# Performance work log

Hardware: AMD Instinct MI355X
Metric: run time of the kernel (lower is better)

Reference implementation:

```python
import jax, jax.numpy as jnp
import numpy as np

NINP, NHID, NOUT = 400, 600, 400
HS = NHID + NOUT          # h_size = nhid + nout
NLEVELS, K, AUX_FREQ = 40, 2, 20
DILATION = [1]


def setup_inputs() -> dict:
    key = jax.random.key(0)
    ks = jax.random.split(key, 6)
    B, T = 8, 256
    bound = 0.01  # matches init_weights normal_(0, 0.01)
    return {
        "X": jax.random.normal(ks[0], (B, NINP, T), jnp.float32),
        "hid": jax.random.normal(ks[1], (B, HS, 1), jnp.float32),
        "cell": jax.random.normal(ks[2], (B, HS, 1), jnp.float32),
        "w1": jax.random.normal(ks[3], (4 * HS, NINP, K), jnp.float32) * bound,
        "w2": jax.random.normal(ks[4], (4 * HS, HS, K), jnp.float32) * bound,
        "b2": jax.random.normal(ks[5], (4 * HS,), jnp.float32) * bound,
    }


def _conv1d(x, w, d):
    # x: [B, Cin, T_padded], w: [Cout, Cin, K] -> [B, Cout, T]
    return jax.lax.conv_general_dilated(
        x, w, window_strides=(1,), padding='VALID', rhs_dilation=(d,),
        dimension_numbers=('NCH', 'OIH', 'NCH'))


def _forward(X, hid, cell, w1, w2, b2):
    B, _, T = X.shape
    ht = jnp.zeros((B, HS, T), X.dtype)
    ct = jnp.zeros((B, HS, T), X.dtype)

    # Input-side convolution is weight-tied and X never changes across levels,
    # so (like the torch dict cache) compute it once per distinct dilation.
    conv1 = {}
    for d in set(DILATION):
        pad = (K - 1) * d
        xp = jnp.pad(X, ((0, 0), (0, 0), (pad, 0)))
        conv1[d] = _conv1d(xp, w1, d)

    aux = []
    for i in range(NLEVELS):
        d = DILATION[i % len(DILATION)]
        pad = (K - 1) * d
        # causal left-pad of the hidden stream, filled with the initial hid
        z1 = jnp.concatenate([jnp.broadcast_to(hid, (B, HS, pad)), ht], axis=2)
        out = conv1[d] + _conv1d(z1, w2, d) + b2[None, :, None]  # [B, 4*HS, T]
        # shifted cell state, first d steps filled with the initial cell
        ct_1 = jnp.concatenate(
            [jnp.broadcast_to(cell, (B, HS, d)), ct[:, :, :-d]], axis=2)
        it = jax.nn.sigmoid(out[:, :HS])
        ot = jax.nn.sigmoid(out[:, HS:2 * HS])
        gt = jnp.tanh(out[:, 2 * HS:3 * HS])
        ft = jax.nn.sigmoid(out[:, 3 * HS:])
        ct = ft * ct_1 + it * gt
        ht = ot * jnp.tanh(ct)
        if i % AUX_FREQ == AUX_FREQ - 1:
            aux.append(ht[:, -NOUT:])  # [B, nout, T]

    out_main = jnp.transpose(ht[:, -NOUT:], (0, 2, 1))            # [B, T, nout]
    hc = (ht[:, :, -1:], ct[:, :, -1:])                            # ([B,HS,1], [B,HS,1])
    aux_outs = jnp.transpose(jnp.stack(aux, axis=0), (1, 0, 3, 2))  # [B, n_aux, T, nout]
    return out_main, hc, aux_outs


def reference(X, hid, cell, w1, w2, b2):
    return _forward(X, hid, cell, w1, w2, b2)
```

## Files before the change

### kernel.cpp

```cpp
#include <hip/hip_runtime.h>
#include <hip/hip_bf16.h>
#include <math.h>

typedef __bf16 bf16;
typedef __bf16 bf16x8 __attribute__((ext_vector_type(8)));
typedef __bf16 bf16x4 __attribute__((ext_vector_type(4)));
typedef float f32x4 __attribute__((ext_vector_type(4)));
typedef unsigned int u32;
typedef u32 u32x4 __attribute__((ext_vector_type(4)));

#define NINP 400
#define HS   1000
#define HP   1024
#define B_   8
#define T_   256
#define NT   2048
#define K2   2048
#define K1   1024
#define M_   4096

#define HT_OFF   819200
#define CT_OFF   827200
#define AUX_OFF  835200

typedef __attribute__((address_space(1))) const void gvoid;
typedef __attribute__((address_space(3))) void lvoid;

__device__ __forceinline__ void async_copy16(void* lds, const void* g) {
  __builtin_amdgcn_global_load_lds((gvoid*)g, (lvoid*)lds, 16, 0, 0);
}

__device__ __forceinline__ float sigm(float x) { return 1.0f / (1.0f + expf(-x)); }


__global__ void repack_w1(const float* __restrict__ w1, bf16* __restrict__ W1q) {
  int idx = blockIdx.x * 256 + threadIdx.x;
  if (idx >= M_ * K1) return;
  int pm = idx >> 10, k = idx & 1023;
  int g = (pm >> 4) & 3;
  int h = (pm >> 7) * 32 + ((pm >> 6) & 1) * 16 + (pm & 15);
  float v = 0.0f;
  if (h < HS) {
    int c = g * HS + h;
    if (k < 512) { if (k < NINP) v = w1[(size_t)c * (NINP * 2) + k * 2 + 0]; }
    else { int j = k - 512; if (j < NINP) v = w1[(size_t)c * (NINP * 2) + j * 2 + 1]; }
  }
  W1q[idx] = (bf16)v;
}

__global__ void repack_w2(const float* __restrict__ w2, bf16* __restrict__ W2q) {
  int idx = blockIdx.x * 256 + threadIdx.x;
  if (idx >= M_ * K2) return;
  int pm = idx >> 11, k = idx & 2047;
  int g = (pm >> 4) & 3;
  int h = (pm >> 7) * 32 + ((pm >> 6) & 1) * 16 + (pm & 15);
  float v = 0.0f;
  if (h < HS) {
    int c = g * HS + h;
    if (k < HP) { if (k < HS) v = w2[(size_t)c * (HS * 2) + k * 2 + 0]; }
    else { int j = k - HP; if (j < HS) v = w2[(size_t)c * (HS * 2) + j * 2 + 1]; }
  }
  W2q[idx] = (bf16)v;
}

__global__ void build_xt(const float* __restrict__ X, bf16* __restrict__ XT) {
  int idx = blockIdx.x * 256 + threadIdx.x;
  if (idx >= NT * K1) return;
  int n = idx >> 10, k = idx & 1023;
  int b = n >> 8, t = n & (T_ - 1);
  float v = 0.0f;
  if (k < 512) { if (k < NINP && t > 0) v = X[((size_t)b * NINP + k) * T_ + t - 1]; }
  else { int j = k - 512; if (j < NINP) v = X[((size_t)b * NINP + j) * T_ + t]; }
  XT[idx] = (bf16)v;
}

__global__ void build_hc(const float* __restrict__ hid, const float* __restrict__ cell,
                         bf16* __restrict__ hidp, float* __restrict__ cellp) {
  int idx = blockIdx.x * 256 + threadIdx.x;
  if (idx >= B_ * HP) return;
  int b = idx >> 10, k = idx & (HP - 1);
  hidp[idx]  = (k < HS) ? (bf16)hid[b * HS + k] : (bf16)0.0f;
  cellp[idx] = (k < HS) ? cell[b * HS + k] : 0.0f;
}


template <bool GATED>
__global__ __launch_bounds__(512, 2) void gemm_step(
    const bf16* __restrict__ A,
    const bf16* __restrict__ Bsrc,
    const bf16* __restrict__ hidp,
    const bf16* __restrict__ CbIn,
    bf16* __restrict__ CbOut,
    const float* __restrict__ b2,
    const bf16* __restrict__ ctprev,
    const float* __restrict__ cellp,
    bf16* __restrict__ ctnew,
    bf16* __restrict__ Hnew,
    int K) {
  __shared__ bf16 As[3][256][64];
  __shared__ bf16 Bs[3][128][64];

  const int tid = threadIdx.x;
  const int lane = tid & 63;
  const int w = tid >> 6;
  const int mh = w >> 1;
  const int nh = w & 1;
  const int dr = lane >> 3, c8 = lane & 7;
  const int swo = ((c8 - dr) & 7) * 8;
  const int quad = lane >> 4, col = lane & 15;

  const int L = blockIdx.y * 16 + blockIdx.x;
  const int bm = (L & 7) * 2 + (L >> 7);
  const int n0 = ((L >> 3) & 15) * 128;

  bf16x4 cb0[4], cb1[4], cb2[4], cb3[4];
  if (GATED) {
#pragma unroll
    for (int nt = 0; nt < 4; ++nt) {
      const int n = n0 + nh * 64 + nt * 16 + col;
      const size_t cb = (size_t)n * 4096 + (size_t)(bm * 256 + mh * 64) + quad * 4;
      cb0[nt] = *(const bf16x4*)&CbIn[cb + 0];
      cb1[nt] = *(const bf16x4*)&CbIn[cb + 16];
      cb2[nt] = *(const bf16x4*)&CbIn[cb + 32];
      cb3[nt] = *(const bf16x4*)&CbIn[cb + 48];
    }
  }

  f32x4 acc[4][4];
#pragma unroll
  for (int i = 0; i < 4; ++i)
#pragma unroll
    for (int j = 0; j < 4; ++j) acc[i][j] = (f32x4){0.f, 0.f, 0.f, 0.f};

  auto stage = [&](int buf, int it2) {
    const int k0 = it2 << 6;
#pragma unroll
    for (int i = 0; i < 4; ++i) {
      const int r = i * 64 + w * 8 + dr;
      async_copy16(&As[buf][i * 64 + w * 8][0],
                   A + (size_t)(bm * 256 + r) * K + k0 + swo);
    }
#pragma unroll
    for (int j = 0; j < 2; ++j) {
      const int r = j * 64 + w * 8 + dr;
      const int n = n0 + r;
      const bf16* bp;
      if (GATED) {
        const int kk = (k0 & (HP - 1)) + swo;
        if (k0 < HP) {
          const int t = n & (T_ - 1);
          bp = (t == 0) ? (hidp + (size_t)(n >> 8) * HP + kk)
                        : (Bsrc + (size_t)(n - 1) * HP + kk);
        } else {
          bp = Bsrc + (size_t)n * HP + kk;
        }
      } else {
        bp = Bsrc + (size_t)n * K + k0 + swo;
      }
      async_copy16(&Bs[buf][j * 64 + w * 8][0], bp);
    }
  };

  const int NIT = K >> 6;
  stage(0, 0);
  stage(1, 1);
  int cur = 0;
  for (int it = 0; it < NIT; ++it) {
    if (it + 1 < NIT) asm volatile("s_waitcnt vmcnt(6)" ::: "memory");
    else              asm volatile("s_waitcnt vmcnt(0)" ::: "memory");
    __builtin_amdgcn_s_barrier();
    if (it + 2 < NIT) {
      int nx = cur + 2; if (nx >= 3) nx -= 3;
      stage(nx, it + 2);
    }
#pragma unroll
    for (int kc = 0; kc < 64; kc += 32) {
      bf16x8 av[4], bv[4];
#pragma unroll
      for (int mt = 0; mt < 4; ++mt) {
        const int rA = mh * 64 + mt * 16 + col;
        av[mt] = *(const bf16x8*)&As[cur][rA][(((kc >> 3) + quad + rA) & 7) * 8];
      }
#pragma unroll
      for (int nt = 0; nt < 4; ++nt) {
        const int rB = nh * 64 + nt * 16 + col;
        bv[nt] = *(const bf16x8*)&Bs[cur][rB][(((kc >> 3) + quad + rB) & 7) * 8];
      }
      __builtin_amdgcn_s_setprio(1);
#pragma unroll
      for (int mt = 0; mt < 4; ++mt)
#pragma unroll
        for (int nt = 0; nt < 4; ++nt)
          acc[mt][nt] = __builtin_amdgcn_mfma_f32_16x16x32_bf16(av[mt], bv[nt], acc[mt][nt], 0, 0, 0);
      __builtin_amdgcn_s_setprio(0);
    }
    cur = (cur == 2) ? 0 : cur + 1;
  }
  __syncthreads();

  if (!GATED) {
    bf16 (*Csh)[256] = (bf16(*)[256])&As[0][0][0];
#pragma unroll
    for (int mt = 0; mt < 4; ++mt) {
#pragma unroll
      for (int nt = 0; nt < 4; ++nt) {
        const int nloc = nh * 64 + nt * 16 + col;
        bf16x4 v;
#pragma unroll
        for (int j = 0; j < 4; ++j) {
          const int h = bm * 64 + mh * 16 + quad * 4 + j;
          const float bias = (h < HS) ? b2[mt * HS + h] : 0.0f;
          v[j] = (bf16)(acc[mt][nt][j] + bias);
        }
        *(bf16x4*)&Csh[nloc][mh * 64 + mt * 16 + quad * 4] = v;
      }
    }
    __syncthreads();
#pragma unroll
    for (int i2 = 0; i2 < 8; ++i2) {
      const int idx = i2 * 512 + tid;
      const int rrow = idx >> 5, off = idx & 31;
      *(u32x4*)&CbOut[(size_t)(n0 + rrow) * 4096 + bm * 256 + off * 8] =
          *(const u32x4*)&Csh[rrow][off * 8];
    }
  } else {
    bf16 (*Hsh)[64] = (bf16(*)[64])&As[0][0][0];
#pragma unroll
    for (int nt = 0; nt < 4; ++nt) {
      const int nloc = nh * 64 + nt * 16 + col;
      const int n = n0 + nloc;
      const int b = n >> 8;
      const int t = n & (T_ - 1);
      bf16x4 hv;
#pragma unroll
      for (int j = 0; j < 4; ++j) {
        const int h = bm * 64 + mh * 16 + quad * 4 + j;
        const float ci = acc[0][nt][j] + (float)cb0[nt][j];
        const float co = acc[1][nt][j] + (float)cb1[nt][j];
        const float cg = acc[2][nt][j] + (float)cb2[nt][j];
        const float cf = acc[3][nt][j] + (float)cb3[nt][j];
        const float ctold = (t == 0) ? cellp[b * HP + h]
                                     : (float)ctprev[(size_t)h * NT + (n - 1)];
        const float cn = sigm(cf) * ctold + sigm(ci) * tanhf(cg);
        ctnew[(size_t)h * NT + n] = (bf16)cn;
        hv[j] = (bf16)(sigm(co) * tanhf(cn));
      }
      *(bf16x4*)&Hsh[nloc][mh * 16 + quad * 4] = hv;
    }
    __syncthreads();
#pragma unroll
    for (int i2 = 0; i2 < 2; ++i2) {
      const int idx = i2 * 512 + tid;
      const int rrow = idx >> 3, off = idx & 7;
      *(u32x4*)&Hnew[(size_t)(n0 + rrow) * HP + bm * 64 + off * 8] =
          *(const u32x4*)&Hsh[rrow][off * 8];
    }
  }
}


__global__ void aux_kernel(const bf16* __restrict__ H, float* __restrict__ out, int s) {
  int idx = blockIdx.x * 256 + threadIdx.x;
  if (idx >= NT * 100) return;
  int n = idx / 100;
  int o = (idx % 100) * 4;
  int b = n >> 8, t = n & (T_ - 1);
  bf16x4 v = *(const bf16x4*)&H[(size_t)n * HP + 600 + o];
  f32x4 f = {(float)v[0], (float)v[1], (float)v[2], (float)v[3]};
  *(f32x4*)&out[AUX_OFF + ((size_t)((b * 2 + s) * T_ + t)) * 400 + o] = f;
}

__global__ void final_kernel(const bf16* __restrict__ H, const bf16* __restrict__ ct,
                             float* __restrict__ out) {
  int idx = blockIdx.x * 256 + threadIdx.x;
  if (idx < NT * 100) {
    int n = idx / 100;
    int o = (idx % 100) * 4;
    int b = n >> 8, t = n & (T_ - 1);
    bf16x4 v = *(const bf16x4*)&H[(size_t)n * HP + 600 + o];
    f32x4 f = {(float)v[0], (float)v[1], (float)v[2], (float)v[3]};
    *(f32x4*)&out[(size_t)n * 400 + o] = f;
    *(f32x4*)&out[AUX_OFF + ((size_t)((b * 2 + 1) * T_ + t)) * 400 + o] = f;
  } else {
    int j = idx - NT * 100;
    if (j < 8000) {
      int b = j / 1000, h = j % 1000;
      out[HT_OFF + j] = (float)H[(size_t)(b * T_ + 255) * HP + h];
    } else if (j < 16000) {
      int jj = j - 8000;
      int b = jj / 1000, h = jj % 1000;
      out[CT_OFF + jj] = (float)ct[(size_t)h * NT + b * T_ + 255];
    }
  }
}


extern "C" void kernel_launch(void* const* d_in, const int* in_sizes, int n_in,
                              void* d_out, int out_size, void* d_ws, size_t ws_size,
                              hipStream_t stream) {
  const float* X    = (const float*)d_in[0];
  const float* hid  = (const float*)d_in[1];
  const float* cell = (const float*)d_in[2];
  const float* w1   = (const float*)d_in[3];
  const float* w2   = (const float*)d_in[4];
  const float* b2   = (const float*)d_in[5];
  float* out = (float*)d_out;

  char* ws = (char*)d_ws;
  size_t off = 0;
  auto alloc = [&](size_t bytes) {
    void* p = ws + off;
    off += (bytes + 255) & ~(size_t)255;
    return p;
  };
  bf16* W2q    = (bf16*)alloc((size_t)M_ * K2 * 2);
  bf16* CbP    = (bf16*)alloc((size_t)NT * M_ * 2);
  bf16* Hb0    = (bf16*)alloc((size_t)NT * HP * 2);
  bf16* ctb0   = (bf16*)alloc((size_t)HP * NT * 2);
  bf16* hidp   = (bf16*)alloc((size_t)B_ * HP * 2);
  float* cellp = (float*)alloc((size_t)B_ * HP * 4);
  char* R = (char*)alloc((size_t)12 * 1024 * 1024);
  bf16* W1q  = (bf16*)R;
  bf16* XT   = (bf16*)(R + (size_t)8 * 1024 * 1024);
  bf16* ctb1 = (bf16*)R;
  bf16* Hb1  = (bf16*)(R + (size_t)4 * 1024 * 1024);

  bf16* Hb[2]  = {Hb0, Hb1};
  bf16* ctb[2] = {ctb0, ctb1};

  hipMemsetAsync(Hb[0], 0, (size_t)NT * HP * 2, stream);
  hipMemsetAsync(ctb[0], 0, (size_t)HP * NT * 2, stream);

  repack_w1<<<(M_ * K1) / 256, 256, 0, stream>>>(w1, W1q);
  repack_w2<<<(M_ * K2) / 256, 256, 0, stream>>>(w2, W2q);
  build_xt<<<(NT * K1) / 256, 256, 0, stream>>>(X, XT);
  build_hc<<<(B_ * HP) / 256, 256, 0, stream>>>(hid, cell, hidp, cellp);

  dim3 grid(16, 16);
  gemm_step<false><<<grid, 512, 0, stream>>>(W1q, XT, nullptr, nullptr, CbP, b2,
                                             nullptr, nullptr, nullptr, nullptr, K1);
  for (int i = 0; i < 40; ++i) {
    int p = i & 1;
    gemm_step<true><<<grid, 512, 0, stream>>>(W2q, Hb[p], hidp, CbP, nullptr, nullptr,
                                              ctb[p], cellp, ctb[p ^ 1], Hb[p ^ 1], K2);
    if (i == 19) aux_kernel<<<800, 256, 0, stream>>>(Hb[p ^ 1], out, 0);
  }
  final_kernel<<<(NT * 100 + 16000 + 255) / 256, 256, 0, stream>>>(Hb[0], ctb[0], out);
}
```

Measured before the change: 2.341 ms.

## Split K-loop into two ping-pong phases interleaving async loads with MFMA

Restructures the GEMM main loop into two half-iterations. Each half reads its LDS fragments, issues half of the next stage's global-to-LDS async copies, synchronises, then runs its MFMA block, with extra barriers and sched_barrier fences between phases. The intent is to spread memory issue across the iteration and keep MFMA work from being interleaved with load issue, hiding latency better. It adds four barriers per iteration, which may cost more than it hides, and the vmcnt(6) wait now depends on a new split of copy counts.

```diff
diff --git a/kernel.cpp b/kernel.cpp
--- a/kernel.cpp
+++ b/kernel.cpp
@@ -132,12 +132,20 @@
 #pragma unroll
     for (int j = 0; j < 4; ++j) acc[i][j] = (f32x4){0.f, 0.f, 0.f, 0.f};
 
-  auto stage = [&](int buf, int it2) {
+  auto stage_h0 = [&](int buf, int it2) {
     const int k0 = it2 << 6;
 #pragma unroll
-    for (int i = 0; i < 4; ++i) {
+    for (int i = 0; i < 3; ++i) {
       const int r = i * 64 + w * 8 + dr;
       async_copy16(&As[buf][i * 64 + w * 8][0],
+                   A + (size_t)(bm * 256 + r) * K + k0 + swo);
+    }
+  };
+  auto stage_h1 = [&](int buf, int it2) {
+    const int k0 = it2 << 6;
+    {
+      const int r = 3 * 64 + w * 8 + dr;
+      async_copy16(&As[buf][3 * 64 + w * 8][0],
                    A + (size_t)(bm * 256 + r) * K + k0 + swo);
     }
 #pragma unroll
@@ -162,30 +170,32 @@
   };
 
   const int NIT = K >> 6;
-  stage(0, 0);
-  stage(1, 1);
+  stage_h0(0, 0); stage_h1(0, 0);
+  stage_h0(1, 1); stage_h1(1, 1);
+  asm volatile("s_waitcnt vmcnt(6)" ::: "memory");
+  __builtin_amdgcn_s_barrier();
+
   int cur = 0;
   for (int it = 0; it < NIT; ++it) {
-    if (it + 1 < NIT) asm volatile("s_waitcnt vmcnt(6)" ::: "memory");
-    else              asm volatile("s_waitcnt vmcnt(0)" ::: "memory");
-    __builtin_amdgcn_s_barrier();
-    if (it + 2 < NIT) {
-      int nx = cur + 2; if (nx >= 3) nx -= 3;
-      stage(nx, it + 2);
-    }
-#pragma unroll
-    for (int kc = 0; kc < 64; kc += 32) {
+    const bool pre = (it + 2 < NIT);
+    int nx = cur + 2; if (nx >= 3) nx -= 3;
+
+    {
       bf16x8 av[4], bv[4];
 #pragma unroll
       for (int mt = 0; mt < 4; ++mt) {
         const int rA = mh * 64 + mt * 16 + col;
-        av[mt] = *(const bf16x8*)&As[cur][rA][(((kc >> 3) + quad + rA) & 7) * 8];
+        av[mt] = *(const bf16x8*)&As[cur][rA][((quad + rA) & 7) * 8];
       }
 #pragma unroll
       for (int nt = 0; nt < 4; ++nt) {
         const int rB = nh * 64 + nt * 16 + col;
-        bv[nt] = *(const bf16x8*)&Bs[cur][rB][(((kc >> 3) + quad + rB) & 7) * 8];
-      }
+        bv[nt] = *(const bf16x8*)&Bs[cur][rB][((quad + rB) & 7) * 8];
+      }
+      if (pre) stage_h0(nx, it + 2);
+      __builtin_amdgcn_s_barrier();
+      asm volatile("s_waitcnt lgkmcnt(0)" ::: "memory");
+      __builtin_amdgcn_sched_barrier(0);
       __builtin_amdgcn_s_setprio(1);
 #pragma unroll
       for (int mt = 0; mt < 4; ++mt)
@@ -193,7 +203,37 @@
         for (int nt = 0; nt < 4; ++nt)
           acc[mt][nt] = __builtin_amdgcn_mfma_f32_16x16x32_bf16(av[mt], bv[nt], acc[mt][nt], 0, 0, 0);
       __builtin_amdgcn_s_setprio(0);
-    }
+      __builtin_amdgcn_s_barrier();
+    }
+
+    {
+      bf16x8 av[4], bv[4];
+#pragma unroll
+      for (int mt = 0; mt < 4; ++mt) {
+        const int rA = mh * 64 + mt * 16 + col;
+        av[mt] = *(const bf16x8*)&As[cur][rA][((4 + quad + rA) & 7) * 8];
+      }
+#pragma unroll
+      for (int nt = 0; nt < 4; ++nt) {
+        const int rB = nh * 64 + nt * 16 + col;
+        bv[nt] = *(const bf16x8*)&Bs[cur][rB][((4 + quad + rB) & 7) * 8];
+      }
+      if (pre) stage_h1(nx, it + 2);
+      if (pre) asm volatile("s_waitcnt vmcnt(6)" ::: "memory");
+      else     asm volatile("s_waitcnt vmcnt(0)" ::: "memory");
+      __builtin_amdgcn_s_barrier();
+      asm volatile("s_waitcnt lgkmcnt(0)" ::: "memory");
+      __builtin_amdgcn_sched_barrier(0);
+      __builtin_amdgcn_s_setprio(1);
+#pragma unroll
+      for (int mt = 0; mt < 4; ++mt)
+#pragma unroll
+        for (int nt = 0; nt < 4; ++nt)
+          acc[mt][nt] = __builtin_amdgcn_mfma_f32_16x16x32_bf16(av[mt], bv[nt], acc[mt][nt], 0, 0, 0);
+      __builtin_amdgcn_s_setprio(0);
+      __builtin_amdgcn_s_barrier();
+    }
+
     cur = (cur == 2) ? 0 : cur + 1;
   }
   __syncthreads();
```

Result: faster. 1.970 ms (-15.8%).
